# Performance work log

Hardware: AMD Instinct MI355X
Metric: run time of the kernel (lower is better)

The kernel has to match this reference:

```python
import jax, jax.numpy as jnp
import numpy as np

B, T, H, U = 64, 4096, 256, 256


def setup_inputs() -> dict:
    key = jax.random.key(0)
    ks = jax.random.split(key, 8)
    s = 1.0 / np.sqrt(H)
    return {
        "query": jax.random.normal(ks[0], (B, H), dtype=jnp.float32),
        "values": jax.random.normal(ks[1], (B, T, H), dtype=jnp.float32),
        "W1": jax.random.normal(ks[2], (H, U), dtype=jnp.float32) * s,
        "b1": jnp.zeros((U,), dtype=jnp.float32),
        "W2": jax.random.normal(ks[3], (H, U), dtype=jnp.float32) * s,
        "b2": jnp.zeros((U,), dtype=jnp.float32),
        "V": jax.random.normal(ks[4], (U, 1), dtype=jnp.float32) * (1.0 / np.sqrt(U)),
        "bV": jnp.zeros((1,), dtype=jnp.float32),
    }


def reference(query, values, W1, b1, W2, b2, V, bV):
    # query: [B,H] -> [B,1,U]; values: [B,T,H] -> [B,T,U]
    q_proj = (query @ W1 + b1)[:, None, :]            # [B,1,U]
    v_proj = jnp.einsum('bth,hu->btu', values, W2) + b2  # [B,T,U]
    score = jnp.tanh(q_proj + v_proj) @ V + bV        # [B,T,1]
    attention_weights = jax.nn.softmax(score, axis=1)  # softmax over T
    context_vector = jnp.sum(attention_weights * values, axis=1)  # [B,H]
    return context_vector, attention_weights
```

## Files before the change

### kernel.cpp

```cpp
#include <hip/hip_runtime.h>
#include <stdint.h>

#define B_ 64
#define T_ 4096
#define H_ 256
#define U_ 256

typedef float f32x4 __attribute__((ext_vector_type(4)));
typedef short short8 __attribute__((ext_vector_type(8)));

__device__ __forceinline__ short bf16rne(float f) {
    uint32_t x = __builtin_bit_cast(uint32_t, f);
    return (short)((x + 0x7FFFu + ((x >> 16) & 1u)) >> 16);
}

__device__ __forceinline__ float fast_tanh(float x) {
    float e = __expf(2.0f * x);
    return 1.0f - 2.0f * __builtin_amdgcn_rcpf(e + 1.0f);
}

__device__ __forceinline__ void wg_barrier_lds() {
    asm volatile("s_waitcnt lgkmcnt(0)" ::: "memory");
    __builtin_amdgcn_sched_barrier(0);
    __builtin_amdgcn_s_barrier();
    __builtin_amdgcn_sched_barrier(0);
}

__global__ __launch_bounds__(256) void k_prep(const float* __restrict__ W2,
                                              uint16_t* __restrict__ w2t,
                                              const float* __restrict__ query,
                                              const float* __restrict__ W1,
                                              const float* __restrict__ b1,
                                              const float* __restrict__ b2,
                                              float* __restrict__ qpc) {
    if (blockIdx.x < 256) {
        int idx = blockIdx.x * 256 + threadIdx.x;
        int h = idx >> 8;
        int u = idx & 255;
        w2t[u * 256 + h] = (uint16_t)bf16rne(W2[idx]);
    } else {
        __shared__ float qrow[H_];
        int b = blockIdx.x - 256, u = threadIdx.x;
        qrow[u] = query[b * H_ + u];
        __syncthreads();
        float acc = b1[u] + b2[u];
#pragma unroll 8
        for (int h = 0; h < H_; ++h) acc += qrow[h] * W1[h * U_ + u];
        qpc[b * U_ + u] = acc;
    }
}

#define TR 32
#define NT 8
__global__ __launch_bounds__(512, 2) void k_main(const float* __restrict__ values,
                                                 const uint16_t* __restrict__ w2t,
                                                 const float* __restrict__ qpc,
                                                 const float* __restrict__ V,
                                                 float* __restrict__ score,
                                                 float* __restrict__ part_O,
                                                 float* __restrict__ part_s) {
    __shared__ __align__(16) char Ab[TR * 512];
    __shared__ float red[TR][9];
    __shared__ float Ored[TR][16][16];
    __shared__ float sred[TR];

    const int tid = threadIdx.x;
    const int wg = blockIdx.x;
    const int b = wg >> 4;
    const int chunk = (wg & 15) * (NT * TR);

    const int w = tid >> 6;
    const int l = tid & 63;
    const int c = l & 15;
    const int g = l >> 4;

    short8 afr[2][8];
#pragma unroll
    for (int s = 0; s < 2; ++s) {
        const uint16_t* ap = w2t + (size_t)(w * 32 + s * 16 + c) * 256 + g * 8;
#pragma unroll
        for (int ks = 0; ks < 8; ++ks) afr[s][ks] = *(const short8*)(ap + ks * 32);
    }
    float qv[2][4], vv[2][4];
#pragma unroll
    for (int s = 0; s < 2; ++s)
#pragma unroll
        for (int r = 0; r < 4; ++r) {
            int u = w * 32 + s * 16 + g * 4 + r;
            qv[s][r] = qpc[b * U_ + u];
            vv[s][r] = V[u];
        }

    const float* vbase = values + (size_t)b * T_ * H_;
    const int srow = tid >> 4;
    const int q = tid & 15;
    const int sswz = (srow & 7) << 4;
    char* wr0 = Ab + srow * 512 + ((q * 16) ^ sswz);
    char* wr1 = Ab + srow * 512 + ((q * 16 + 256) ^ sswz);
    const float* sbase = vbase + (size_t)srow * H_ + q * 8;

    f32x4 vt[3][4];
    float Oacc[16];
#pragma unroll
    for (int j = 0; j < 16; ++j) Oacc[j] = 0.f;
    float sacc = 0.f;

    {
        const float* nb0 = sbase + (size_t)chunk * H_;
        vt[0][0] = *(const f32x4*)(nb0);       vt[0][1] = *(const f32x4*)(nb0 + 4);
        vt[0][2] = *(const f32x4*)(nb0 + 128); vt[0][3] = *(const f32x4*)(nb0 + 132);
        const float* nb1 = sbase + (size_t)(chunk + TR) * H_;
        vt[1][0] = *(const f32x4*)(nb1);       vt[1][1] = *(const f32x4*)(nb1 + 4);
        vt[1][2] = *(const f32x4*)(nb1 + 128); vt[1][3] = *(const f32x4*)(nb1 + 132);
    }

#pragma unroll
    for (int t = 0; t < NT; ++t) {
        const int cs = t % 3;
        const int os = (t + 2) % 3;
        wg_barrier_lds();
        {
            short8 s0, s1;
            s0[0] = bf16rne(vt[cs][0][0]); s0[1] = bf16rne(vt[cs][0][1]);
            s0[2] = bf16rne(vt[cs][0][2]); s0[3] = bf16rne(vt[cs][0][3]);
            s0[4] = bf16rne(vt[cs][1][0]); s0[5] = bf16rne(vt[cs][1][1]);
            s0[6] = bf16rne(vt[cs][1][2]); s0[7] = bf16rne(vt[cs][1][3]);
            s1[0] = bf16rne(vt[cs][2][0]); s1[1] = bf16rne(vt[cs][2][1]);
            s1[2] = bf16rne(vt[cs][2][2]); s1[3] = bf16rne(vt[cs][2][3]);
            s1[4] = bf16rne(vt[cs][3][0]); s1[5] = bf16rne(vt[cs][3][1]);
            s1[6] = bf16rne(vt[cs][3][2]); s1[7] = bf16rne(vt[cs][3][3]);
            *(short8*)wr0 = s0;
            *(short8*)wr1 = s1;
        }
        if (t > 0) {
            float ssum = 0.f;
#pragma unroll
            for (int j = 0; j < 8; ++j) ssum += red[srow][j];
            float wgt = __expf(ssum);
            if (q == 0) {
                sacc += wgt;
                score[(size_t)b * T_ + chunk + (t - 1) * TR + srow] = ssum;
            }
#pragma unroll
            for (int vj = 0; vj < 4; ++vj)
#pragma unroll
                for (int j = 0; j < 4; ++j)
                    Oacc[vj * 4 + j] += wgt * vt[os][vj][j];
        }
        if (t + 2 < NT) {
            const float* nb = sbase + (size_t)(chunk + (t + 2) * TR) * H_;
            vt[os][0] = *(const f32x4*)(nb);       vt[os][1] = *(const f32x4*)(nb + 4);
            vt[os][2] = *(const f32x4*)(nb + 128); vt[os][3] = *(const f32x4*)(nb + 132);
        }
        wg_barrier_lds();
#pragma unroll
        for (int sub = 0; sub < 2; ++sub) {
            const char* rp = Ab + (sub * 16 + c) * 512;
            const int swz = (c & 7) << 4;
            f32x4 acc0 = (f32x4)(0.0f);
            f32x4 acc1 = (f32x4)(0.0f);
#pragma unroll
            for (int ks = 0; ks < 8; ++ks) {
                short8 bf = *(const short8*)(rp + ((ks * 64 + g * 16) ^ swz));
                acc0 = __builtin_amdgcn_mfma_f32_16x16x32_bf16(afr[0][ks], bf, acc0, 0, 0, 0);
                acc1 = __builtin_amdgcn_mfma_f32_16x16x32_bf16(afr[1][ks], bf, acc1, 0, 0, 0);
            }
            float p = 0.f;
#pragma unroll
            for (int r = 0; r < 4; ++r) {
                p += fast_tanh(acc0[r] + qv[0][r]) * vv[0][r];
                p += fast_tanh(acc1[r] + qv[1][r]) * vv[1][r];
            }
            p += __shfl_xor(p, 16, 64);
            p += __shfl_xor(p, 32, 64);
            if (g == 0) red[sub * 16 + c][w] = p;
        }
    }
    __syncthreads();
    {
        const int fs = (NT - 1) % 3;
        float ssum = 0.f;
#pragma unroll
        for (int j = 0; j < 8; ++j) ssum += red[srow][j];
        float wgt = __expf(ssum);
        if (q == 0) {
            sacc += wgt;
            score[(size_t)b * T_ + chunk + (NT - 1) * TR + srow] = ssum;
        }
#pragma unroll
        for (int vj = 0; vj < 4; ++vj)
#pragma unroll
            for (int j = 0; j < 4; ++j)
                Oacc[vj * 4 + j] += wgt * vt[fs][vj][j];
    }
#pragma unroll
    for (int j = 0; j < 16; ++j) Ored[srow][q][j] = Oacc[j];
    if (q == 0) sred[srow] = sacc;
    __syncthreads();
    if (tid < 256) {
        int col = tid;
        int qq, jj;
        if (col < 128) { qq = col >> 3; jj = col & 7; }
        else           { qq = (col - 128) >> 3; jj = 8 + (col & 7); }
        float o = 0.f;
#pragma unroll
        for (int s = 0; s < TR; ++s) o += Ored[s][qq][jj];
        part_O[(size_t)wg * 256 + col] = o;
    }
    if (tid == 0) {
        float sb = 0.f;
#pragma unroll
        for (int s = 0; s < TR; ++s) sb += sred[s];
        part_s[wg] = sb;
    }
}

__global__ __launch_bounds__(256) void k_fin(const float* __restrict__ part_O,
                                             const float* __restrict__ part_s,
                                             const float* __restrict__ score,
                                             float* __restrict__ ctx,
                                             float* __restrict__ weights) {
    int b = blockIdx.x >> 3;
    int j = blockIdx.x & 7;
    int col = threadIdx.x;
    float sb = 0.f;
#pragma unroll
    for (int ch = 0; ch < 16; ++ch) sb += part_s[b * 16 + ch];
    float inv = 1.0f / sb;
    if (j == 0) {
        float o = 0.f;
#pragma unroll
        for (int ch = 0; ch < 16; ++ch) o += part_O[(size_t)(b * 16 + ch) * 256 + col];
        ctx[b * H_ + col] = o * inv;
    }
#pragma unroll
    for (int i = 0; i < 2; ++i) {
        int idx = j * 512 + i * 256 + col;
        float s = score[(size_t)b * T_ + idx];
        weights[(size_t)b * T_ + idx] = __expf(s) * inv;
    }
}

extern "C" void kernel_launch(void* const* d_in, const int* in_sizes, int n_in,
                              void* d_out, int out_size, void* d_ws, size_t ws_size,
                              hipStream_t stream) {
    const float* query  = (const float*)d_in[0];
    const float* values = (const float*)d_in[1];
    const float* W1     = (const float*)d_in[2];
    const float* b1     = (const float*)d_in[3];
    const float* W2     = (const float*)d_in[4];
    const float* b2     = (const float*)d_in[5];
    const float* V      = (const float*)d_in[6];

    float* out = (float*)d_out;
    float* ctx = out;
    float* weights = out + B_ * H_;

    char* ws = (char*)d_ws;
    uint16_t* w2t   = (uint16_t*)ws;
    float* qpc      = (float*)(ws + 131072);
    float* scorebuf = (float*)(ws + 131072 + 65536);
    float* part_O   = (float*)(ws + 131072 + 65536 + 1048576);
    float* part_s   = (float*)(ws + 131072 + 65536 + 2097152);

    k_prep<<<dim3(320), dim3(256), 0, stream>>>(W2, w2t, query, W1, b1, b2, qpc);
    k_main<<<dim3(1024), dim3(512), 0, stream>>>(values, w2t, qpc, V, scorebuf,
                                                 part_O, part_s);
    k_fin<<<dim3(512), dim3(256), 0, stream>>>(part_O, part_s, scorebuf, ctx, weights);
}
```

Measured before the change: 94.54 us.

## Drop triple-buffered value registers, reload tiles for weighting, raise occupancy

Replaces the three-deep register buffer of value tiles with a single buffer. The tile used for the weighted context sum is now re-read from global memory (likely an L2 hit) instead of being held in registers. This frees registers so launch bounds can request 4 waves-per-SIMD occupancy instead of 2. The cost is an extra global read per tile and a prefetch distance cut to one tile, which may expose more load latency.

Result: slower. 287.3 us (+203.9%).

```diff
diff --git a/kernel.cpp b/kernel.cpp
--- a/kernel.cpp
+++ b/kernel.cpp
@@ -52,7 +52,7 @@
 
 #define TR 32
 #define NT 8
-__global__ __launch_bounds__(512, 2) void k_main(const float* __restrict__ values,
+__global__ __launch_bounds__(512, 4) void k_main(const float* __restrict__ values,
                                                  const uint16_t* __restrict__ w2t,
                                                  const float* __restrict__ qpc,
                                                  const float* __restrict__ V,
@@ -99,40 +99,38 @@
     char* wr1 = Ab + srow * 512 + ((q * 16 + 256) ^ sswz);
     const float* sbase = vbase + (size_t)srow * H_ + q * 8;
 
-    f32x4 vt[3][4];
+    f32x4 vt0, vt1, vt2, vt3;
     float Oacc[16];
 #pragma unroll
     for (int j = 0; j < 16; ++j) Oacc[j] = 0.f;
     float sacc = 0.f;
 
     {
-        const float* nb0 = sbase + (size_t)chunk * H_;
-        vt[0][0] = *(const f32x4*)(nb0);       vt[0][1] = *(const f32x4*)(nb0 + 4);
-        vt[0][2] = *(const f32x4*)(nb0 + 128); vt[0][3] = *(const f32x4*)(nb0 + 132);
-        const float* nb1 = sbase + (size_t)(chunk + TR) * H_;
-        vt[1][0] = *(const f32x4*)(nb1);       vt[1][1] = *(const f32x4*)(nb1 + 4);
-        vt[1][2] = *(const f32x4*)(nb1 + 128); vt[1][3] = *(const f32x4*)(nb1 + 132);
+        const float* nb = sbase + (size_t)chunk * H_;
+        vt0 = *(const f32x4*)(nb);       vt1 = *(const f32x4*)(nb + 4);
+        vt2 = *(const f32x4*)(nb + 128); vt3 = *(const f32x4*)(nb + 132);
     }
 
 #pragma unroll
     for (int t = 0; t < NT; ++t) {
-        const int cs = t % 3;
-        const int os = (t + 2) % 3;
         wg_barrier_lds();
         {
             short8 s0, s1;
-            s0[0] = bf16rne(vt[cs][0][0]); s0[1] = bf16rne(vt[cs][0][1]);
-            s0[2] = bf16rne(vt[cs][0][2]); s0[3] = bf16rne(vt[cs][0][3]);
-            s0[4] = bf16rne(vt[cs][1][0]); s0[5] = bf16rne(vt[cs][1][1]);
-            s0[6] = bf16rne(vt[cs][1][2]); s0[7] = bf16rne(vt[cs][1][3]);
-            s1[0] = bf16rne(vt[cs][2][0]); s1[1] = bf16rne(vt[cs][2][1]);
-            s1[2] = bf16rne(vt[cs][2][2]); s1[3] = bf16rne(vt[cs][2][3]);
-            s1[4] = bf16rne(vt[cs][3][0]); s1[5] = bf16rne(vt[cs][3][1]);
-            s1[6] = bf16rne(vt[cs][3][2]); s1[7] = bf16rne(vt[cs][3][3]);
+            s0[0] = bf16rne(vt0[0]); s0[1] = bf16rne(vt0[1]);
+            s0[2] = bf16rne(vt0[2]); s0[3] = bf16rne(vt0[3]);
+            s0[4] = bf16rne(vt1[0]); s0[5] = bf16rne(vt1[1]);
+            s0[6] = bf16rne(vt1[2]); s0[7] = bf16rne(vt1[3]);
+            s1[0] = bf16rne(vt2[0]); s1[1] = bf16rne(vt2[1]);
+            s1[2] = bf16rne(vt2[2]); s1[3] = bf16rne(vt2[3]);
+            s1[4] = bf16rne(vt3[0]); s1[5] = bf16rne(vt3[1]);
+            s1[6] = bf16rne(vt3[2]); s1[7] = bf16rne(vt3[3]);
             *(short8*)wr0 = s0;
             *(short8*)wr1 = s1;
         }
         if (t > 0) {
+            const float* rb = sbase + (size_t)(chunk + (t - 1) * TR) * H_;
+            vt0 = *(const f32x4*)(rb);       vt1 = *(const f32x4*)(rb + 4);
+            vt2 = *(const f32x4*)(rb + 128); vt3 = *(const f32x4*)(rb + 132);
             float ssum = 0.f;
 #pragma unroll
             for (int j = 0; j < 8; ++j) ssum += red[srow][j];
@@ -142,15 +140,17 @@
                 score[(size_t)b * T_ + chunk + (t - 1) * TR + srow] = ssum;
             }
 #pragma unroll
-            for (int vj = 0; vj < 4; ++vj)
-#pragma unroll
-                for (int j = 0; j < 4; ++j)
-                    Oacc[vj * 4 + j] += wgt * vt[os][vj][j];
-        }
-        if (t + 2 < NT) {
-            const float* nb = sbase + (size_t)(chunk + (t + 2) * TR) * H_;
-            vt[os][0] = *(const f32x4*)(nb);       vt[os][1] = *(const f32x4*)(nb + 4);
-            vt[os][2] = *(const f32x4*)(nb + 128); vt[os][3] = *(const f32x4*)(nb + 132);
+            for (int j = 0; j < 4; ++j) {
+                Oacc[j]      += wgt * vt0[j];
+                Oacc[4 + j]  += wgt * vt1[j];
+                Oacc[8 + j]  += wgt * vt2[j];
+                Oacc[12 + j] += wgt * vt3[j];
+            }
+        }
+        if (t + 1 < NT) {
+            const float* nb = sbase + (size_t)(chunk + (t + 1) * TR) * H_;
+            vt0 = *(const f32x4*)(nb);       vt1 = *(const f32x4*)(nb + 4);
+            vt2 = *(const f32x4*)(nb + 128); vt3 = *(const f32x4*)(nb + 132);
         }
         wg_barrier_lds();
 #pragma unroll
@@ -178,7 +178,9 @@
     }
     __syncthreads();
     {
-        const int fs = (NT - 1) % 3;
+        const float* rb = sbase + (size_t)(chunk + (NT - 1) * TR) * H_;
+        vt0 = *(const f32x4*)(rb);       vt1 = *(const f32x4*)(rb + 4);
+        vt2 = *(const f32x4*)(rb + 128); vt3 = *(const f32x4*)(rb + 132);
         float ssum = 0.f;
 #pragma unroll
         for (int j = 0; j < 8; ++j) ssum += red[srow][j];
@@ -188,10 +190,12 @@
             score[(size_t)b * T_ + chunk + (NT - 1) * TR + srow] = ssum;
         }
 #pragma unroll
-        for (int vj = 0; vj < 4; ++vj)
-#pragma unroll
-            for (int j = 0; j < 4; ++j)
-                Oacc[vj * 4 + j] += wgt * vt[fs][vj][j];
+        for (int j = 0; j < 4; ++j) {
+            Oacc[j]      += wgt * vt0[j];
+            Oacc[4 + j]  += wgt * vt1[j];
+            Oacc[8 + j]  += wgt * vt2[j];
+            Oacc[12 + j] += wgt * vt3[j];
+        }
     }
 #pragma unroll
     for (int j = 0; j < 16; ++j) Ored[srow][q][j] = Oacc[j];
```

## Remap value tile loads per wave, re-read rows for context, use packed bf16 convert

Applied to the files above, without the earlier changes.

Each wave now loads four full 256-wide rows with 16-byte coalesced loads and converts them with the hardware packed bf16 instruction, replacing the 16-threads-per-row split and the software rounding. The three-slot register ring is dropped. Rows are instead reloaded from global memory (cache-resident) for the weighted context accumulation, with the exp weights broadcast by shuffles. This cuts registers and LDS for the partial reduction, at the cost of reading each value tile twice and possibly exposing latency from the single-slot prefetch.

New measurement: 105.0 us. 1.11x slower.

```diff
diff --git a/kernel.cpp b/kernel.cpp
--- a/kernel.cpp
+++ b/kernel.cpp
@@ -8,6 +8,7 @@
 
 typedef float f32x4 __attribute__((ext_vector_type(4)));
 typedef short short8 __attribute__((ext_vector_type(8)));
+typedef unsigned int uint2v __attribute__((ext_vector_type(2)));
 
 __device__ __forceinline__ short bf16rne(float f) {
     uint32_t x = __builtin_bit_cast(uint32_t, f);
@@ -24,6 +25,14 @@
     __builtin_amdgcn_sched_barrier(0);
     __builtin_amdgcn_s_barrier();
     __builtin_amdgcn_sched_barrier(0);
+}
+
+__device__ __forceinline__ uint2v pack_bf16x4(const f32x4 a) {
+    uint32_t w0, w1;
+    asm("v_cvt_pk_bf16_f32 %0, %1, %2" : "=v"(w0) : "v"(a[0]), "v"(a[1]));
+    asm("v_cvt_pk_bf16_f32 %0, %1, %2" : "=v"(w1) : "v"(a[2]), "v"(a[3]));
+    uint2v r; r[0] = w0; r[1] = w1;
+    return r;
 }
 
 __global__ __launch_bounds__(256) void k_prep(const float* __restrict__ W2,
@@ -60,24 +69,24 @@
                                                  float* __restrict__ part_O,
                                                  float* __restrict__ part_s) {
     __shared__ __align__(16) char Ab[TR * 512];
-    __shared__ float red[TR][9];
-    __shared__ float Ored[TR][16][16];
-    __shared__ float sred[TR];
+    __shared__ __align__(16) float red[TR][12];
+    __shared__ __align__(16) float Ored[8][260];
+    __shared__ float sred[8];
 
     const int tid = threadIdx.x;
     const int wg = blockIdx.x;
     const int b = wg >> 4;
     const int chunk = (wg & 15) * (NT * TR);
 
-    const int w = tid >> 6;
-    const int l = tid & 63;
-    const int c = l & 15;
-    const int g = l >> 4;
+    const int wv = tid >> 6;
+    const int p = tid & 63;
+    const int c = p & 15;
+    const int g = p >> 4;
 
     short8 afr[2][8];
 #pragma unroll
     for (int s = 0; s < 2; ++s) {
-        const uint16_t* ap = w2t + (size_t)(w * 32 + s * 16 + c) * 256 + g * 8;
+        const uint16_t* ap = w2t + (size_t)(wv * 32 + s * 16 + c) * 256 + g * 8;
 #pragma unroll
         for (int ks = 0; ks < 8; ++ks) afr[s][ks] = *(const short8*)(ap + ks * 32);
     }
@@ -86,71 +95,69 @@
     for (int s = 0; s < 2; ++s)
 #pragma unroll
         for (int r = 0; r < 4; ++r) {
-            int u = w * 32 + s * 16 + g * 4 + r;
+            int u = wv * 32 + s * 16 + g * 4 + r;
             qv[s][r] = qpc[b * U_ + u];
             vv[s][r] = V[u];
         }
 
     const float* vbase = values + (size_t)b * T_ * H_;
-    const int srow = tid >> 4;
-    const int q = tid & 15;
-    const int sswz = (srow & 7) << 4;
-    char* wr0 = Ab + srow * 512 + ((q * 16) ^ sswz);
-    char* wr1 = Ab + srow * 512 + ((q * 16 + 256) ^ sswz);
-    const float* sbase = vbase + (size_t)srow * H_ + q * 8;
-
-    f32x4 vt[3][4];
-    float Oacc[16];
-#pragma unroll
-    for (int j = 0; j < 16; ++j) Oacc[j] = 0.f;
+    const int r0 = wv * 4;
+    char* st0 = Ab + (r0 + 0) * 512 + ((p * 8) ^ (((r0 + 0) & 7) << 4));
+    char* st1 = Ab + (r0 + 1) * 512 + ((p * 8) ^ (((r0 + 1) & 7) << 4));
+    char* st2 = Ab + (r0 + 2) * 512 + ((p * 8) ^ (((r0 + 2) & 7) << 4));
+    char* st3 = Ab + (r0 + 3) * 512 + ((p * 8) ^ (((r0 + 3) & 7) << 4));
+    const float* lb = vbase + (size_t)r0 * H_ + p * 4;
+
+    f32x4 vt0, vt1, vt2, vt3;
+    float Oacc[4] = {0.f, 0.f, 0.f, 0.f};
     float sacc = 0.f;
 
     {
-        const float* nb0 = sbase + (size_t)chunk * H_;
-        vt[0][0] = *(const f32x4*)(nb0);       vt[0][1] = *(const f32x4*)(nb0 + 4);
-        vt[0][2] = *(const f32x4*)(nb0 + 128); vt[0][3] = *(const f32x4*)(nb0 + 132);
-        const float* nb1 = sbase + (size_t)(chunk + TR) * H_;
-        vt[1][0] = *(const f32x4*)(nb1);       vt[1][1] = *(const f32x4*)(nb1 + 4);
-        vt[1][2] = *(const f32x4*)(nb1 + 128); vt[1][3] = *(const f32x4*)(nb1 + 132);
+        const float* nb = lb + (size_t)chunk * H_;
+        vt0 = *(const f32x4*)(nb);
+        vt1 = *(const f32x4*)(nb + H_);
+        vt2 = *(const f32x4*)(nb + 2 * H_);
+        vt3 = *(const f32x4*)(nb + 3 * H_);
     }
 
 #pragma unroll
     for (int t = 0; t < NT; ++t) {
-        const int cs = t % 3;
-        const int os = (t + 2) % 3;
         wg_barrier_lds();
-        {
-            short8 s0, s1;
-            s0[0] = bf16rne(vt[cs][0][0]); s0[1] = bf16rne(vt[cs][0][1]);
-            s0[2] = bf16rne(vt[cs][0][2]); s0[3] = bf16rne(vt[cs][0][3]);
-            s0[4] = bf16rne(vt[cs][1][0]); s0[5] = bf16rne(vt[cs][1][1]);
-            s0[6] = bf16rne(vt[cs][1][2]); s0[7] = bf16rne(vt[cs][1][3]);
-            s1[0] = bf16rne(vt[cs][2][0]); s1[1] = bf16rne(vt[cs][2][1]);
-            s1[2] = bf16rne(vt[cs][2][2]); s1[3] = bf16rne(vt[cs][2][3]);
-            s1[4] = bf16rne(vt[cs][3][0]); s1[5] = bf16rne(vt[cs][3][1]);
-            s1[6] = bf16rne(vt[cs][3][2]); s1[7] = bf16rne(vt[cs][3][3]);
-            *(short8*)wr0 = s0;
-            *(short8*)wr1 = s1;
-        }
+        *(uint2v*)st0 = pack_bf16x4(vt0);
+        *(uint2v*)st1 = pack_bf16x4(vt1);
+        *(uint2v*)st2 = pack_bf16x4(vt2);
+        *(uint2v*)st3 = pack_bf16x4(vt3);
         if (t > 0) {
-            float ssum = 0.f;
-#pragma unroll
-            for (int j = 0; j < 8; ++j) ssum += red[srow][j];
-            float wgt = __expf(ssum);
-            if (q == 0) {
-                sacc += wgt;
-                score[(size_t)b * T_ + chunk + (t - 1) * TR + srow] = ssum;
+            const float* rb = lb + (size_t)(chunk + (t - 1) * TR) * H_;
+            vt0 = *(const f32x4*)(rb);
+            vt1 = *(const f32x4*)(rb + H_);
+            vt2 = *(const f32x4*)(rb + 2 * H_);
+            vt3 = *(const f32x4*)(rb + 3 * H_);
+            float pexp = 0.f;
+            if (p < 4) {
+                const float* rr = &red[r0 + p][0];
+                f32x4 s0 = *(const f32x4*)(rr);
+                f32x4 s1 = *(const f32x4*)(rr + 4);
+                float ssum = ((s0[0] + s0[1]) + (s0[2] + s0[3])) +
+                             ((s1[0] + s1[1]) + (s1[2] + s1[3]));
+                pexp = __expf(ssum);
+                sacc += pexp;
+                score[(size_t)b * T_ + chunk + (t - 1) * TR + r0 + p] = ssum;
             }
-#pragma unroll
-            for (int vj = 0; vj < 4; ++vj)
-#pragma unroll
-                for (int j = 0; j < 4; ++j)
-                    Oacc[vj * 4 + j] += wgt * vt[os][vj][j];
-        }
-        if (t + 2 < NT) {
-            const float* nb = sbase + (size_t)(chunk + (t + 2) * TR) * H_;
-            vt[os][0] = *(const f32x4*)(nb);       vt[os][1] = *(const f32x4*)(nb + 4);
-            vt[os][2] = *(const f32x4*)(nb + 128); vt[os][3] = *(const f32x4*)(nb + 132);
+            float w0 = __shfl(pexp, 0, 64);
+            float w1 = __shfl(pexp, 1, 64);
+            float w2 = __shfl(pexp, 2, 64);
+            float w3 = __shfl(pexp, 3, 64);
+#pragma unroll
+            for (int j = 0; j < 4; ++j)
+                Oacc[j] += w0 * vt0[j] + w1 * vt1[j] + w2 * vt2[j] + w3 * vt3[j];
+        }
+        if (t + 1 < NT) {
+            const float* nb = lb + (size_t)(chunk + (t + 1) * TR) * H_;
+            vt0 = *(const f32x4*)(nb);
+            vt1 = *(const f32x4*)(nb + H_);
+            vt2 = *(const f32x4*)(nb + 2 * H_);
+            vt3 = *(const f32x4*)(nb + 3 * H_);
         }
         wg_barrier_lds();
 #pragma unroll
@@ -165,52 +172,58 @@
                 acc0 = __builtin_amdgcn_mfma_f32_16x16x32_bf16(afr[0][ks], bf, acc0, 0, 0, 0);
                 acc1 = __builtin_amdgcn_mfma_f32_16x16x32_bf16(afr[1][ks], bf, acc1, 0, 0, 0);
             }
-            float p = 0.f;
+            float ps = 0.f;
 #pragma unroll
             for (int r = 0; r < 4; ++r) {
-                p += fast_tanh(acc0[r] + qv[0][r]) * vv[0][r];
-                p += fast_tanh(acc1[r] + qv[1][r]) * vv[1][r];
+                ps += fast_tanh(acc0[r] + qv[0][r]) * vv[0][r];
+                ps += fast_tanh(acc1[r] + qv[1][r]) * vv[1][r];
             }
-            p += __shfl_xor(p, 16, 64);
-            p += __shfl_xor(p, 32, 64);
-            if (g == 0) red[sub * 16 + c][w] = p;
+            ps += __shfl_xor(ps, 16, 64);
+            ps += __shfl_xor(ps, 32, 64);
+            if (g == 0) red[sub * 16 + c][wv] = ps;
         }
     }
     __syncthreads();
     {
-        const int fs = (NT - 1) % 3;
-        float ssum = 0.f;
-#pragma unroll
-        for (int j = 0; j < 8; ++j) ssum += red[srow][j];
-        float wgt = __expf(ssum);
-        if (q == 0) {
-            sacc += wgt;
-            score[(size_t)b * T_ + chunk + (NT - 1) * TR + srow] = ssum;
-        }
-#pragma unroll
-        for (int vj = 0; vj < 4; ++vj)
-#pragma unroll
-            for (int j = 0; j < 4; ++j)
-                Oacc[vj * 4 + j] += wgt * vt[fs][vj][j];
-    }
-#pragma unroll
-    for (int j = 0; j < 16; ++j) Ored[srow][q][j] = Oacc[j];
-    if (q == 0) sred[srow] = sacc;
+        const float* rb = lb + (size_t)(chunk + (NT - 1) * TR) * H_;
+        vt0 = *(const f32x4*)(rb);
+        vt1 = *(const f32x4*)(rb + H_);
+        vt2 = *(const f32x4*)(rb + 2 * H_);
+        vt3 = *(const f32x4*)(rb + 3 * H_);
+        float pexp = 0.f;
+        if (p < 4) {
+            const float* rr = &red[r0 + p][0];
+            f32x4 s0 = *(const f32x4*)(rr);
+            f32x4 s1 = *(const f32x4*)(rr + 4);
+            float ssum = ((s0[0] + s0[1]) + (s0[2] + s0[3])) +
+                         ((s1[0] + s1[1]) + (s1[2] + s1[3]));
+            pexp = __expf(ssum);
+            sacc += pexp;
+            score[(size_t)b * T_ + chunk + (NT - 1) * TR + r0 + p] = ssum;
+        }
+        float w0 = __shfl(pexp, 0, 64);
+        float w1 = __shfl(pexp, 1, 64);
+        float w2 = __shfl(pexp, 2, 64);
+        float w3 = __shfl(pexp, 3, 64);
+#pragma unroll
+        for (int j = 0; j < 4; ++j)
+            Oacc[j] += w0 * vt0[j] + w1 * vt1[j] + w2 * vt2[j] + w3 * vt3[j];
+    }
+    *(f32x4*)(&Ored[wv][p * 4]) = *(f32x4*)Oacc;
+    sacc += __shfl_xor(sacc, 1, 64);
+    sacc += __shfl_xor(sacc, 2, 64);
+    if (p == 0) sred[wv] = sacc;
     __syncthreads();
     if (tid < 256) {
-        int col = tid;
-        int qq, jj;
-        if (col < 128) { qq = col >> 3; jj = col & 7; }
-        else           { qq = (col - 128) >> 3; jj = 8 + (col & 7); }
         float o = 0.f;
 #pragma unroll
-        for (int s = 0; s < TR; ++s) o += Ored[s][qq][jj];
-        part_O[(size_t)wg * 256 + col] = o;
+        for (int j = 0; j < 8; ++j) o += Ored[j][tid];
+        part_O[(size_t)wg * 256 + tid] = o;
     }
     if (tid == 0) {
         float sb = 0.f;
 #pragma unroll
-        for (int s = 0; s < TR; ++s) sb += sred[s];
+        for (int j = 0; j < 8; ++j) sb += sred[j];
         part_s[wg] = sb;
     }
 }
```
